# Performance work log

Hardware: AMD Instinct MI355X
Metric: run time of the kernel (lower is better)

The kernel has to match this reference:

```python
import jax, jax.numpy as jnp
import numpy as np

D_MODEL = 1024
NUM_HEADS = 16
D_K = D_MODEL // NUM_HEADS
B, S = 2, 2048


def setup_inputs() -> dict:
    key = jax.random.key(0)
    ks = jax.random.split(key, 4)
    scale = 1.0 / np.sqrt(D_MODEL)
    x = jax.random.normal(ks[0], (B, S, D_MODEL), dtype=jnp.float32)
    w_qkv = jax.random.normal(ks[1], (D_MODEL, 3 * D_MODEL), dtype=jnp.float32) * scale
    b_qkv = jnp.zeros((3 * D_MODEL,), dtype=jnp.float32)
    w_out = jax.random.normal(ks[2], (D_MODEL, D_MODEL), dtype=jnp.float32) * scale
    b_out = jnp.zeros((D_MODEL,), dtype=jnp.float32)
    # causal mask: 1 where attention is allowed (j <= i), 0 elsewhere
    mask = jnp.tril(jnp.ones((S, S), dtype=jnp.int32))
    return {"x": x, "mask": mask, "w_qkv": w_qkv, "b_qkv": b_qkv,
            "w_out": w_out, "b_out": b_out}


def reference(x, mask, w_qkv, b_qkv, w_out, b_out):
    Bb, Ss, C = x.shape
    qkv = x @ w_qkv + b_qkv                      # [B,S,3C]
    q, k, v = jnp.split(qkv, 3, axis=-1)
    def split_heads(t):
        return t.reshape(Bb, Ss, NUM_HEADS, D_K).transpose(0, 2, 1, 3)  # [B,H,S,Dk]
    q, k, v = split_heads(q), split_heads(k), split_heads(v)
    scores = jnp.einsum('bhqd,bhkd->bhqk', q, k) / jnp.sqrt(jnp.float32(D_K))
    scores = jnp.where(mask == 0, -jnp.inf, scores)
    weights = jax.nn.softmax(scores, axis=-1)
    weights = jnp.nan_to_num(weights, nan=0.0)   # matches torch.nan_to_num
    attn = jnp.einsum('bhqk,bhkd->bhqd', weights, v)
    attn = attn.transpose(0, 2, 1, 3).reshape(Bb, Ss, C)
    return attn @ w_out + b_out
```

## Files before the change

### kernel.cpp

```cpp
#include <hip/hip_runtime.h>
#include <hip/hip_bf16.h>

#define D_MODEL 1024
#define NUM_HEADS 16
#define D_K 64
#define BATCH 2
#define SEQ 2048

typedef __attribute__((ext_vector_type(8))) short bf16x8;
typedef __attribute__((ext_vector_type(4))) float f32x4;

union P16 { int4 i4; ushort u[8]; };
union FU { float f; unsigned int u; };

__device__ __forceinline__ float bf2f(ushort u) {
    union { unsigned int i; float f; } c; c.i = ((unsigned int)u) << 16; return c.f;
}
__device__ __forceinline__ ushort f2bf(float f) {
    union { float f; unsigned int i; } c; c.f = f;
    unsigned int x = c.i;
    return (ushort)((x + 0x7fff + ((x >> 16) & 1)) >> 16);
}

__device__ __forceinline__ bool wave_detect_f32(const ushort* x) {
    ushort u = x[2 * (threadIdx.x & 63)];
    int e = (u >> 7) & 0xFF;
    unsigned long long bl = __ballot(e >= 100 && e <= 141);
    return __popcll(bl) < 32;
}

__global__ __launch_bounds__(256)
void prep_all(const ushort* __restrict__ x, const void* __restrict__ Wq,
              const void* __restrict__ Wo, ushort* __restrict__ xb,
              ushort* __restrict__ WqT, ushort* __restrict__ WoT,
              int* __restrict__ flag)
{
    const bool f32 = wave_detect_f32(x);
    const int bx = blockIdx.x, tx = threadIdx.x;
    if (bx == 0 && tx == 0) flag[0] = f32 ? 1 : 0;

    if (bx >= 1024) {
        if (!f32) return;
        int i = ((bx - 1024) * 256 + tx) * 8;
        const float* f = (const float*)x + i;
        float4 a = *(const float4*)f, b = *(const float4*)(f + 4);
        P16 r;
        r.u[0] = f2bf(a.x); r.u[1] = f2bf(a.y); r.u[2] = f2bf(a.z); r.u[3] = f2bf(a.w);
        r.u[4] = f2bf(b.x); r.u[5] = f2bf(b.y); r.u[6] = f2bf(b.z); r.u[7] = f2bf(b.w);
        *(int4*)(xb + i) = r.i4;
        return;
    }

    __shared__ ushort t[64][72];
    const int nb = bx & 63, kb = bx >> 6;
    const void* W; ushort* WT; int N, n0;
    if (nb < 48) { W = Wq; WT = WqT; N = 3 * D_MODEL; n0 = nb * 64; }
    else         { W = Wo; WT = WoT; N = D_MODEL;     n0 = (nb - 48) * 64; }
    const int k0 = kb * 64, K = D_MODEL;
    #pragma unroll
    for (int p = 0; p < 16; ++p) {
        int r = p * 4 + (tx >> 6), c = tx & 63;
        float v = f32 ? ((const float*)W)[(size_t)(k0 + r) * N + n0 + c]
                      : bf2f(((const ushort*)W)[(size_t)(k0 + r) * N + n0 + c]);
        t[r][c] = f2bf(v);
    }
    __syncthreads();
    #pragma unroll
    for (int p = 0; p < 16; ++p) {
        int nn = p * 4 + (tx >> 6), kk = tx & 63;
        WT[(size_t)(n0 + nn) * K + k0 + kk] = t[kk][nn];
    }
}

template<int MODE>
__global__ __launch_bounds__(256)
void gemm128(const void* __restrict__ Araw, const ushort* __restrict__ Aconv,
             const ushort* __restrict__ WT, const void* __restrict__ bias,
             void* __restrict__ out, int N, int K, const int* __restrict__ flag)
{
    __shared__ ushort As[128 * 32];
    __shared__ ushort Bs[128 * 32];

    const int f = *flag;
    const ushort* A = (MODE == 1) ? (f ? Aconv : (const ushort*)Araw) : Aconv;

    const int tid = threadIdx.x;
    const int w = tid >> 6, lane = tid & 63;
    const int ln = lane & 15, quad = lane >> 4;
    const int m0 = blockIdx.y * 128, n0 = blockIdx.x * 128;
    const int wm = (w >> 1) * 64, wn = (w & 1) * 64;

    const int s0 = w * 128 + lane, s1 = s0 + 64;
    const int ar0 = s0 >> 2, ak0 = ((s0 & 3) ^ ((ar0 >> 1) & 3)) * 8;
    const int ar1 = s1 >> 2, ak1 = ((s1 & 3) ^ ((ar1 >> 1) & 3)) * 8;
    const size_t aoff0 = (size_t)(m0 + ar0) * K + ak0;
    const size_t aoff1 = (size_t)(m0 + ar1) * K + ak1;
    const size_t boff0 = (size_t)(n0 + ar0) * K + ak0;
    const size_t boff1 = (size_t)(n0 + ar1) * K + ak1;
    ushort* alds0 = As + s0 * 8;
    ushort* alds1 = As + s1 * 8;
    ushort* blds0 = Bs + s0 * 8;
    ushort* blds1 = Bs + s1 * 8;

    const int physc = (quad ^ ((ln >> 1) & 3)) * 8;

    f32x4 acc[4][4] = {};

    int4 a0 = *(const int4*)(A + aoff0);
    int4 a1 = *(const int4*)(A + aoff1);
    int4 b0 = *(const int4*)(WT + boff0);
    int4 b1 = *(const int4*)(WT + boff1);

    for (int k0c = 0; k0c < K; k0c += 32) {
        __syncthreads();
        *(int4*)alds0 = a0;
        *(int4*)alds1 = a1;
        *(int4*)blds0 = b0;
        *(int4*)blds1 = b1;
        __syncthreads();

        if (k0c + 32 < K) {
            a0 = *(const int4*)(A + aoff0 + k0c + 32);
            a1 = *(const int4*)(A + aoff1 + k0c + 32);
            b0 = *(const int4*)(WT + boff0 + k0c + 32);
            b1 = *(const int4*)(WT + boff1 + k0c + 32);
        }

        bf16x8 af[4], bf[4];
        #pragma unroll
        for (int t = 0; t < 4; ++t) {
            af[t] = *(const bf16x8*)(As + (wm + t * 16 + ln) * 32 + physc);
            bf[t] = *(const bf16x8*)(Bs + (wn + t * 16 + ln) * 32 + physc);
        }
        #pragma unroll
        for (int mi = 0; mi < 4; ++mi)
            #pragma unroll
            for (int ni = 0; ni < 4; ++ni)
                acc[mi][ni] = __builtin_amdgcn_mfma_f32_16x16x32_bf16(
                    af[mi], bf[ni], acc[mi][ni], 0, 0, 0);
    }

    #pragma unroll
    for (int mi = 0; mi < 4; ++mi) {
        #pragma unroll
        for (int ni = 0; ni < 4; ++ni) {
            int col = n0 + wn + ni * 16 + ln;
            float bb = f ? ((const float*)bias)[col] : bf2f(((const ushort*)bias)[col]);
            #pragma unroll
            for (int r = 0; r < 4; ++r) {
                int row = m0 + wm + mi * 16 + quad * 4 + r;
                float v = acc[mi][ni][r] + bb;
                if (MODE == 0 && f) ((float*)out)[(size_t)row * N + col] = v;
                else                ((ushort*)out)[(size_t)row * N + col] = f2bf(v);
            }
        }
    }
}

__global__ __launch_bounds__(256)
void flash_attn7(const ushort* __restrict__ qkv, ushort* __restrict__ attn)
{
    __shared__ ushort Ks[64][72];
    __shared__ ushort Vs[64][72];
    __shared__ ushort QPs[128][72];

    const int tid  = threadIdx.x;
    const int wave = tid >> 6, lane = tid & 63;
    const int ln   = lane & 15, quad = lane >> 4;
    const int pg   = wave >> 1, ww = wave & 1;
    const int bh   = blockIdx.x;
    const int ky   = blockIdx.y;
    const int k    = (ky < 8) ? ky : 23 - ky;
    const int xx   = 2 * k + pg;
    const int b    = bh >> 4, hh = bh & (NUM_HEADS - 1);
    const int W3   = 3 * D_MODEL;
    const size_t hbase = (size_t)b * SEQ * W3 + hh * D_K;

    const int q0A = 32 * (63 - xx), q0B = 32 * xx;
    const int ntA = 32 - k, ntB = k + 1;

    const int qrr = tid >> 1, qcol = (tid & 1) * 32;
    const int ksr = tid >> 2, ksc = (tid & 3) * 16;
    const int vp  = tid & 31, vg = (tid >> 5) * 8;

    {
        const int qpg = qrr >> 6, qmt = (qrr >> 5) & 1, ql = qrr & 31;
        const int qxx = 2 * k + qpg;
        const int grow = qmt ? (32 * qxx + ql) : (32 * (63 - qxx) + ql);
        const ushort* src = qkv + hbase + (size_t)grow * W3 + qcol;
        #pragma unroll
        for (int h = 0; h < 4; ++h) {
            P16 v; v.i4 = *(const int4*)(src + h * 8);
            #pragma unroll
            for (int e = 0; e < 8; ++e) v.u[e] = f2bf(bf2f(v.u[e]) * 0.18033688011f);
            *(int4*)(&QPs[qrr][qcol + h * 8]) = v.i4;
        }
    }
    __syncthreads();
    bf16x8 qf[2][2];
    #pragma unroll
    for (int mt = 0; mt < 2; ++mt)
        #pragma unroll
        for (int s = 0; s < 2; ++s)
            qf[mt][s] = *(const bf16x8*)(&QPs[pg * 64 + mt * 32 + ww * 16 + ln][s * 32 + quad * 8]);

    f32x4 acc_o[2][4] = {};
    f32x4 acc_l[2] = {};

    bf16x8 ones8;
    #pragma unroll
    for (int e = 0; e < 8; ++e) ones8[e] = (short)0x3F80;

    const ushort* Kbase = qkv + hbase + D_MODEL;
    const ushort* Vbase = qkv + hbase + 2 * D_MODEL;

    int4 kreg[2], vreg[2];
    {
        const ushort* ksrc = Kbase + (size_t)ksr * W3 + ksc;
        kreg[0] = *(const int4*)(ksrc);
        kreg[1] = *(const int4*)(ksrc + 8);
        vreg[0] = *(const int4*)(Vbase + (size_t)(2 * vp)     * W3 + vg);
        vreg[1] = *(const int4*)(Vbase + (size_t)(2 * vp + 1) * W3 + vg);
    }

    for (int jt = 0; jt < ntA; ++jt) {
        const int j0 = jt * 64;
        const bool doB = (jt < ntB);
        __syncthreads();

        *(int4*)(&Ks[ksr][ksc])     = kreg[0];
        *(int4*)(&Ks[ksr][ksc + 8]) = kreg[1];
        {
            P16 v0, v1; v0.i4 = vreg[0]; v1.i4 = vreg[1];
            #pragma unroll
            for (int e = 0; e < 8; ++e) {
                unsigned int pack = (unsigned int)v0.u[e] | ((unsigned int)v1.u[e] << 16);
                *(unsigned int*)(&Vs[vg + e][2 * vp]) = pack;
            }
        }
        __syncthreads();

        if (jt + 1 < ntA) {
            const int jn = j0 + 64;
            const ushort* ksrc = Kbase + (size_t)(jn + ksr) * W3 + ksc;
            kreg[0] = *(const int4*)(ksrc);
            kreg[1] = *(const int4*)(ksrc + 8);
            vreg[0] = *(const int4*)(Vbase + (size_t)(jn + 2 * vp)     * W3 + vg);
            vreg[1] = *(const int4*)(Vbase + (size_t)(jn + 2 * vp + 1) * W3 + vg);
        }

        f32x4 sa[2][4];
        #pragma unroll
        for (int t = 0; t < 4; ++t) {
            bf16x8 k0 = *(const bf16x8*)(&Ks[t * 16 + ln][quad * 8]);
            bf16x8 k1 = *(const bf16x8*)(&Ks[t * 16 + ln][32 + quad * 8]);
            {
                f32x4 z = {};
                z = __builtin_amdgcn_mfma_f32_16x16x32_bf16(qf[0][0], k0, z, 0, 0, 0);
                z = __builtin_amdgcn_mfma_f32_16x16x32_bf16(qf[0][1], k1, z, 0, 0, 0);
                sa[0][t] = z;
            }
            if (doB) {
                f32x4 z = {};
                z = __builtin_amdgcn_mfma_f32_16x16x32_bf16(qf[1][0], k0, z, 0, 0, 0);
                z = __builtin_amdgcn_mfma_f32_16x16x32_bf16(qf[1][1], k1, z, 0, 0, 0);
                sa[1][t] = z;
            }
        }

        if (jt == ntA - 1) {
            const int rowb = q0A + ww * 16 + quad * 4;
            #pragma unroll
            for (int t = 0; t < 4; ++t)
                #pragma unroll
                for (int r = 0; r < 4; ++r)
                    if (j0 + t * 16 + ln > rowb + r) sa[0][t][r] = -1e30f;
        }
        if (doB && jt == ntB - 1) {
            const int rowb = q0B + ww * 16 + quad * 4;
            #pragma unroll
            for (int t = 0; t < 4; ++t)
                #pragma unroll
                for (int r = 0; r < 4; ++r)
                    if (j0 + t * 16 + ln > rowb + r) sa[1][t][r] = -1e30f;
        }

        const int lnx = ln ^ ((quad & 1) * 8);
        #pragma unroll
        for (int mt = 0; mt < 2; ++mt) {
            if (mt && !doB) break;
            #pragma unroll
            for (int r = 0; r < 4; ++r) {
                const int prow = pg * 64 + mt * 32 + ww * 16 + quad * 4 + r;
                #pragma unroll
                for (int t = 0; t < 4; ++t) {
                    FU cc; cc.f = exp2f(sa[mt][t][r]);
                    QPs[prow][((t ^ (quad >> 1)) * 16) + lnx] = (ushort)(cc.u >> 16);
                }
            }
        }

        #pragma unroll
        for (int s = 0; s < 2; ++s) {
            const int pcol = s * 32 + ((quad ^ ((ln >> 2) & 3)) * 8);
            bf16x8 pf0 = *(const bf16x8*)(&QPs[pg * 64 + ww * 16 + ln][pcol]);
            bf16x8 pf1;
            if (doB) pf1 = *(const bf16x8*)(&QPs[pg * 64 + 32 + ww * 16 + ln][pcol]);
            #pragma unroll
            for (int t = 0; t < 4; ++t) {
                bf16x8 vf = *(const bf16x8*)(&Vs[t * 16 + ln][s * 32 + quad * 8]);
                acc_o[0][t] = __builtin_amdgcn_mfma_f32_16x16x32_bf16(pf0, vf, acc_o[0][t], 0, 0, 0);
                if (doB)
                    acc_o[1][t] = __builtin_amdgcn_mfma_f32_16x16x32_bf16(pf1, vf, acc_o[1][t], 0, 0, 0);
            }
            acc_l[0] = __builtin_amdgcn_mfma_f32_16x16x32_bf16(pf0, ones8, acc_l[0], 0, 0, 0);
            if (doB)
                acc_l[1] = __builtin_amdgcn_mfma_f32_16x16x32_bf16(pf1, ones8, acc_l[1], 0, 0, 0);
        }
    }

    #pragma unroll
    for (int mt = 0; mt < 2; ++mt) {
        const int q0 = mt ? q0B : q0A;
        #pragma unroll
        for (int r = 0; r < 4; ++r) {
            float inv = 1.0f / acc_l[mt][r];
            int i = q0 + ww * 16 + quad * 4 + r;
            size_t rowoff = ((size_t)(b * SEQ + i)) * D_MODEL + hh * D_K;
            #pragma unroll
            for (int t = 0; t < 4; ++t)
                attn[rowoff + t * 16 + ln] = f2bf(acc_o[mt][t][r] * inv);
        }
    }
}

extern "C" void kernel_launch(void* const* d_in, const int* in_sizes, int n_in,
                              void* d_out, int out_size, void* d_ws, size_t ws_size,
                              hipStream_t stream)
{
    const void* x     = d_in[0];
    const void* w_qkv = d_in[2];
    const void* b_qkv = d_in[3];
    const void* w_out = d_in[4];
    const void* b_out = d_in[5];

    char* ws = (char*)d_ws;
    int*    flag   = (int*)ws;                  size_t off = 256;
    ushort* WqkvT  = (ushort*)(ws + off);       off += (size_t)3 * D_MODEL * D_MODEL * 2;
    ushort* WoutT  = (ushort*)(ws + off);       off += (size_t)D_MODEL * D_MODEL * 2;
    ushort* qkv_ws = (ushort*)(ws + off);       off += (size_t)BATCH * SEQ * 3 * D_MODEL * 2;
    ushort* xb     = (ushort*)(ws + off);
    ushort* attn_ws = xb;

    const int M = BATCH * SEQ;

    prep_all<<<3072, 256, 0, stream>>>((const ushort*)x, w_qkv, w_out,
                                       xb, WqkvT, WoutT, flag);

    gemm128<1><<<dim3(3 * D_MODEL / 128, M / 128), 256, 0, stream>>>(
        x, xb, WqkvT, b_qkv, qkv_ws, 3 * D_MODEL, D_MODEL, flag);

    dim3 ga(BATCH * NUM_HEADS, 16);
    flash_attn7<<<ga, 256, 0, stream>>>(qkv_ws, attn_ws);

    gemm128<0><<<dim3(D_MODEL / 128, M / 128), 256, 0, stream>>>(
        attn_ws, attn_ws, WoutT, b_out, d_out, D_MODEL, D_MODEL, flag);
}
```

Before: 218.0 us.

## Double-buffer LDS tiles in GEMM and flash attention to halve barriers

Both the GEMM kernel and the attention kernel now keep two shared-memory buffers for their K-loop tiles. The next tile is stored to the other buffer while the current one is consumed, and global loads are issued two tiles ahead. Each iteration now needs one barrier instead of two, which cuts synchronisation stalls and lets stores overlap with MFMA work. In exchange, shared-memory use per block roughly doubles for the staged tiles, which may reduce occupancy.

```diff
diff --git a/kernel.cpp b/kernel.cpp
--- a/kernel.cpp
+++ b/kernel.cpp
@@ -78,8 +78,8 @@
              const ushort* __restrict__ WT, const void* __restrict__ bias,
              void* __restrict__ out, int N, int K, const int* __restrict__ flag)
 {
-    __shared__ ushort As[128 * 32];
-    __shared__ ushort Bs[128 * 32];
+    __shared__ ushort As[2][128 * 32];
+    __shared__ ushort Bs[2][128 * 32];
 
     const int f = *flag;
     const ushort* A = (MODE == 1) ? (f ? Aconv : (const ushort*)Araw) : Aconv;
@@ -97,40 +97,47 @@
     const size_t aoff1 = (size_t)(m0 + ar1) * K + ak1;
     const size_t boff0 = (size_t)(n0 + ar0) * K + ak0;
     const size_t boff1 = (size_t)(n0 + ar1) * K + ak1;
-    ushort* alds0 = As + s0 * 8;
-    ushort* alds1 = As + s1 * 8;
-    ushort* blds0 = Bs + s0 * 8;
-    ushort* blds1 = Bs + s1 * 8;
 
     const int physc = (quad ^ ((ln >> 1) & 3)) * 8;
 
     f32x4 acc[4][4] = {};
 
+    const int nk = K >> 5;
     int4 a0 = *(const int4*)(A + aoff0);
     int4 a1 = *(const int4*)(A + aoff1);
     int4 b0 = *(const int4*)(WT + boff0);
     int4 b1 = *(const int4*)(WT + boff1);
-
-    for (int k0c = 0; k0c < K; k0c += 32) {
-        __syncthreads();
-        *(int4*)alds0 = a0;
-        *(int4*)alds1 = a1;
-        *(int4*)blds0 = b0;
-        *(int4*)blds1 = b1;
-        __syncthreads();
-
-        if (k0c + 32 < K) {
-            a0 = *(const int4*)(A + aoff0 + k0c + 32);
-            a1 = *(const int4*)(A + aoff1 + k0c + 32);
-            b0 = *(const int4*)(WT + boff0 + k0c + 32);
-            b1 = *(const int4*)(WT + boff1 + k0c + 32);
+    *(int4*)(As[0] + s0 * 8) = a0;
+    *(int4*)(As[0] + s1 * 8) = a1;
+    *(int4*)(Bs[0] + s0 * 8) = b0;
+    *(int4*)(Bs[0] + s1 * 8) = b1;
+    a0 = *(const int4*)(A + aoff0 + 32);
+    a1 = *(const int4*)(A + aoff1 + 32);
+    b0 = *(const int4*)(WT + boff0 + 32);
+    b1 = *(const int4*)(WT + boff1 + 32);
+    __syncthreads();
+
+    for (int kt = 0; kt < nk; ++kt) {
+        const int cur = kt & 1;
+        if (kt + 1 < nk) {
+            *(int4*)(As[1 - cur] + s0 * 8) = a0;
+            *(int4*)(As[1 - cur] + s1 * 8) = a1;
+            *(int4*)(Bs[1 - cur] + s0 * 8) = b0;
+            *(int4*)(Bs[1 - cur] + s1 * 8) = b1;
+        }
+        if (kt + 2 < nk) {
+            const int kc = (kt + 2) * 32;
+            a0 = *(const int4*)(A + aoff0 + kc);
+            a1 = *(const int4*)(A + aoff1 + kc);
+            b0 = *(const int4*)(WT + boff0 + kc);
+            b1 = *(const int4*)(WT + boff1 + kc);
         }
 
         bf16x8 af[4], bf[4];
         #pragma unroll
         for (int t = 0; t < 4; ++t) {
-            af[t] = *(const bf16x8*)(As + (wm + t * 16 + ln) * 32 + physc);
-            bf[t] = *(const bf16x8*)(Bs + (wn + t * 16 + ln) * 32 + physc);
+            af[t] = *(const bf16x8*)(As[cur] + (wm + t * 16 + ln) * 32 + physc);
+            bf[t] = *(const bf16x8*)(Bs[cur] + (wn + t * 16 + ln) * 32 + physc);
         }
         #pragma unroll
         for (int mi = 0; mi < 4; ++mi)
@@ -138,6 +145,7 @@
             for (int ni = 0; ni < 4; ++ni)
                 acc[mi][ni] = __builtin_amdgcn_mfma_f32_16x16x32_bf16(
                     af[mi], bf[ni], acc[mi][ni], 0, 0, 0);
+        __syncthreads();
     }
 
     #pragma unroll
@@ -158,10 +166,10 @@
 }
 
 __global__ __launch_bounds__(256)
-void flash_attn7(const ushort* __restrict__ qkv, ushort* __restrict__ attn)
+void flash_attn8(const ushort* __restrict__ qkv, ushort* __restrict__ attn)
 {
-    __shared__ ushort Ks[64][72];
-    __shared__ ushort Vs[64][72];
+    __shared__ ushort Ks[2][64][72];
+    __shared__ ushort Vs[2][64][72];
     __shared__ ushort QPs[128][72];
 
     const int tid  = threadIdx.x;
@@ -196,20 +204,6 @@
             *(int4*)(&QPs[qrr][qcol + h * 8]) = v.i4;
         }
     }
-    __syncthreads();
-    bf16x8 qf[2][2];
-    #pragma unroll
-    for (int mt = 0; mt < 2; ++mt)
-        #pragma unroll
-        for (int s = 0; s < 2; ++s)
-            qf[mt][s] = *(const bf16x8*)(&QPs[pg * 64 + mt * 32 + ww * 16 + ln][s * 32 + quad * 8]);
-
-    f32x4 acc_o[2][4] = {};
-    f32x4 acc_l[2] = {};
-
-    bf16x8 ones8;
-    #pragma unroll
-    for (int e = 0; e < 8; ++e) ones8[e] = (short)0x3F80;
 
     const ushort* Kbase = qkv + hbase + D_MODEL;
     const ushort* Vbase = qkv + hbase + 2 * D_MODEL;
@@ -222,26 +216,56 @@
         vreg[0] = *(const int4*)(Vbase + (size_t)(2 * vp)     * W3 + vg);
         vreg[1] = *(const int4*)(Vbase + (size_t)(2 * vp + 1) * W3 + vg);
     }
+    *(int4*)(&Ks[0][ksr][ksc])     = kreg[0];
+    *(int4*)(&Ks[0][ksr][ksc + 8]) = kreg[1];
+    {
+        P16 v0, v1; v0.i4 = vreg[0]; v1.i4 = vreg[1];
+        #pragma unroll
+        for (int e = 0; e < 8; ++e) {
+            unsigned int pack = (unsigned int)v0.u[e] | ((unsigned int)v1.u[e] << 16);
+            *(unsigned int*)(&Vs[0][vg + e][2 * vp]) = pack;
+        }
+    }
+    {
+        const ushort* ksrc = Kbase + (size_t)(64 + ksr) * W3 + ksc;
+        kreg[0] = *(const int4*)(ksrc);
+        kreg[1] = *(const int4*)(ksrc + 8);
+        vreg[0] = *(const int4*)(Vbase + (size_t)(64 + 2 * vp)     * W3 + vg);
+        vreg[1] = *(const int4*)(Vbase + (size_t)(64 + 2 * vp + 1) * W3 + vg);
+    }
+    __syncthreads();
+
+    bf16x8 qf[2][2];
+    #pragma unroll
+    for (int mt = 0; mt < 2; ++mt)
+        #pragma unroll
+        for (int s = 0; s < 2; ++s)
+            qf[mt][s] = *(const bf16x8*)(&QPs[pg * 64 + mt * 32 + ww * 16 + ln][s * 32 + quad * 8]);
+
+    f32x4 acc_o[2][4] = {};
+    f32x4 acc_l[2] = {};
+
+    bf16x8 ones8;
+    #pragma unroll
+    for (int e = 0; e < 8; ++e) ones8[e] = (short)0x3F80;
 
     for (int jt = 0; jt < ntA; ++jt) {
+        const int cur = jt & 1;
         const int j0 = jt * 64;
         const bool doB = (jt < ntB);
-        __syncthreads();
-
-        *(int4*)(&Ks[ksr][ksc])     = kreg[0];
-        *(int4*)(&Ks[ksr][ksc + 8]) = kreg[1];
-        {
+
+        if (jt + 1 < ntA) {
+            *(int4*)(&Ks[1 - cur][ksr][ksc])     = kreg[0];
+            *(int4*)(&Ks[1 - cur][ksr][ksc + 8]) = kreg[1];
             P16 v0, v1; v0.i4 = vreg[0]; v1.i4 = vreg[1];
             #pragma unroll
             for (int e = 0; e < 8; ++e) {
                 unsigned int pack = (unsigned int)v0.u[e] | ((unsigned int)v1.u[e] << 16);
-                *(unsigned int*)(&Vs[vg + e][2 * vp]) = pack;
-            }
-        }
-        __syncthreads();
-
-        if (jt + 1 < ntA) {
-            const int jn = j0 + 64;
+                *(unsigned int*)(&Vs[1 - cur][vg + e][2 * vp]) = pack;
+            }
+        }
+        if (jt + 2 < ntA) {
+            const int jn = j0 + 128;
             const ushort* ksrc = Kbase + (size_t)(jn + ksr) * W3 + ksc;
             kreg[0] = *(const int4*)(ksrc);
             kreg[1] = *(const int4*)(ksrc + 8);
@@ -252,8 +276,8 @@
         f32x4 sa[2][4];
         #pragma unroll
         for (int t = 0; t < 4; ++t) {
-            bf16x8 k0 = *(const bf16x8*)(&Ks[t * 16 + ln][quad * 8]);
-            bf16x8 k1 = *(const bf16x8*)(&Ks[t * 16 + ln][32 + quad * 8]);
+            bf16x8 k0 = *(const bf16x8*)(&Ks[cur][t * 16 + ln][quad * 8]);
+            bf16x8 k1 = *(const bf16x8*)(&Ks[cur][t * 16 + ln][32 + quad * 8]);
             {
                 f32x4 z = {};
                 z = __builtin_amdgcn_mfma_f32_16x16x32_bf16(qf[0][0], k0, z, 0, 0, 0);
@@ -308,7 +332,7 @@
             if (doB) pf1 = *(const bf16x8*)(&QPs[pg * 64 + 32 + ww * 16 + ln][pcol]);
             #pragma unroll
             for (int t = 0; t < 4; ++t) {
-                bf16x8 vf = *(const bf16x8*)(&Vs[t * 16 + ln][s * 32 + quad * 8]);
+                bf16x8 vf = *(const bf16x8*)(&Vs[cur][t * 16 + ln][s * 32 + quad * 8]);
                 acc_o[0][t] = __builtin_amdgcn_mfma_f32_16x16x32_bf16(pf0, vf, acc_o[0][t], 0, 0, 0);
                 if (doB)
                     acc_o[1][t] = __builtin_amdgcn_mfma_f32_16x16x32_bf16(pf1, vf, acc_o[1][t], 0, 0, 0);
@@ -317,6 +341,8 @@
             if (doB)
                 acc_l[1] = __builtin_amdgcn_mfma_f32_16x16x32_bf16(pf1, ones8, acc_l[1], 0, 0, 0);
         }
+
+        __syncthreads();
     }
 
     #pragma unroll
@@ -361,7 +387,7 @@
         x, xb, WqkvT, b_qkv, qkv_ws, 3 * D_MODEL, D_MODEL, flag);
 
     dim3 ga(BATCH * NUM_HEADS, 16);
-    flash_attn7<<<ga, 256, 0, stream>>>(qkv_ws, attn_ws);
+    flash_attn8<<<ga, 256, 0, stream>>>(qkv_ws, attn_ws);
 
     gemm128<0><<<dim3(D_MODEL / 128, M / 128), 256, 0, stream>>>(
         attn_ws, attn_ws, WoutT, b_out, d_out, D_MODEL, D_MODEL, flag);
```

Measured after the change: 232.1 us. +6.5%, slower.
